# Kernel optimization log

Measured on AMD Instinct MI355X. Metric: run time of the kernel, lower is better.

## Reference

```python
import jax, jax.numpy as jnp
import numpy as np

BETA = 0.5        # membrane decay (from source)
THRESHOLD = 1.0   # snn.Leaky default
ALPHA = 2.0       # ATan surrogate default slope (snntorch)


@jax.custom_vjp
def spike_fn(v):
    # Heaviside spike: 1 where membrane - threshold > 0
    return (v > 0).astype(v.dtype)


def _spike_fwd(v):
    return spike_fn(v), v


def _spike_bwd(v, g):
    # snntorch ATan surrogate gradient: (alpha/2) / (1 + (pi/2*alpha*v)^2)
    grad = (ALPHA / 2.0) / (1.0 + (jnp.pi / 2.0 * ALPHA * v) ** 2)
    return (g * grad,)


spike_fn.defvjp(_spike_fwd, _spike_bwd)


def setup_inputs() -> dict:
    key = jax.random.key(0)
    # x: [T, B, N] = [num_steps, batch, neurons]
    x = jax.random.normal(key, (128, 64, 4096), dtype=jnp.float32)
    return {"x": x}


def reference(x):
    # snntorch Leaky with init_hidden=True, reset_mechanism='subtract':
    #   reset_t = H(mem_{t-1} - thr)
    #   mem_t   = beta*mem_{t-1} + x_t - reset_t*thr
    #   spk_t   = H(mem_t - thr)
    mem0 = jnp.zeros(x.shape[1:], dtype=x.dtype)

    def step(mem, xt):
        reset = spike_fn(mem - THRESHOLD)
        mem_new = BETA * mem + xt - reset * THRESHOLD
        spk = spike_fn(mem_new - THRESHOLD)
        return mem_new, spk

    _, spk_rec = jax.lax.scan(step, mem0, x)  # spk_rec: [T, B, N]
    return spk_rec
```

## Files before the change

### kernel.cpp

```cpp
#include <hip/hip_runtime.h>


#define T_STEPS 128
#define T_HALF 64
#define D 8

__device__ __forceinline__ float4 lif_step(float4& mem, const float4 v) {
    mem.x = 0.5f * mem.x + v.x - (mem.x > 1.0f ? 1.0f : 0.0f);
    mem.y = 0.5f * mem.y + v.y - (mem.y > 1.0f ? 1.0f : 0.0f);
    mem.z = 0.5f * mem.z + v.z - (mem.z > 1.0f ? 1.0f : 0.0f);
    mem.w = 0.5f * mem.w + v.w - (mem.w > 1.0f ? 1.0f : 0.0f);
    float4 s;
    s.x = mem.x > 1.0f ? 1.0f : 0.0f;
    s.y = mem.y > 1.0f ? 1.0f : 0.0f;
    s.z = mem.z > 1.0f ? 1.0f : 0.0f;
    s.w = mem.w > 1.0f ? 1.0f : 0.0f;
    return s;
}

__global__ __launch_bounds__(256) void snn_leaky_fwd(const float4* __restrict__ x,
                                                     float4* __restrict__ out,
                                                     int n4) {
    const int chunk = blockIdx.x & 255;
    const int phase = blockIdx.x >> 8;
    const int col = chunk * 256 + threadIdx.x;

    const float4* xp = x + col;
    float4* op = out + col;

    float4 buf[D];
    float4 mem = make_float4(0.f, 0.f, 0.f, 0.f);

#pragma unroll
    for (int u = 0; u < D; ++u) buf[u] = xp[(size_t)u * n4];

    if (phase == 0) {
#pragma unroll
        for (int t = 0; t < T_HALF; ++t) {
            const float4 v = buf[t % D];
            if (t + D < T_HALF) buf[t % D] = xp[(size_t)(t + D) * n4];
            const float4 s = lif_step(mem, v);
            op[(size_t)t * n4] = s;
        }
    } else {
#pragma unroll
        for (int t = 0; t < T_HALF; ++t) {
            const float4 v = buf[t % D];
            buf[t % D] = xp[(size_t)(t + D) * n4];
            (void)lif_step(mem, v);
        }
#pragma unroll
        for (int t = T_HALF; t < T_STEPS; ++t) {
            const float4 v = buf[t % D];
            if (t + D < T_STEPS) buf[t % D] = xp[(size_t)(t + D) * n4];
            const float4 s = lif_step(mem, v);
            op[(size_t)t * n4] = s;
        }
    }
}

extern "C" void kernel_launch(void* const* d_in, const int* in_sizes, int n_in,
                              void* d_out, int out_size, void* d_ws, size_t ws_size,
                              hipStream_t stream) {
    const float4* x = (const float4*)d_in[0];
    float4* out = (float4*)d_out;

    const int total = in_sizes[0];
    const int n4 = total / T_STEPS / 4;

    snn_leaky_fwd<<<512, 256, 0, stream>>>(x, out, n4);
}
```

Before: 224.4 us.

## Replace split-phase recompute with single pass paced by cross-block atomic barriers

Drops the two-phase scheme, where the second half of blocks re-ran the first 64 timesteps just to rebuild membrane state. Each of 256 blocks now walks all 128 steps. Blocks are held roughly in lockstep every 8 steps by a global atomic counter with bounded spinning, so memory traffic stays time-aligned across the device. This removes the redundant reads and compute, but halves the grid and adds 15 barrier rounds of atomic spinning plus a memset before launch.

```diff
diff --git a/kernel.cpp b/kernel.cpp
--- a/kernel.cpp
+++ b/kernel.cpp
@@ -2,8 +2,12 @@
 
 
 #define T_STEPS 128
-#define T_HALF 64
 #define D 8
+#define KWIN 8
+#define NWIN (T_STEPS / KWIN)
+#define NBLK 256
+#define BLKT 256
+#define SPIN_CAP 20000
 
 __device__ __forceinline__ float4 lif_step(float4& mem, const float4 v) {
     mem.x = 0.5f * mem.x + v.x - (mem.x > 1.0f ? 1.0f : 0.0f);
@@ -18,13 +22,11 @@
     return s;
 }
 
-__global__ __launch_bounds__(256) void snn_leaky_fwd(const float4* __restrict__ x,
-                                                     float4* __restrict__ out,
-                                                     int n4) {
-    const int chunk = blockIdx.x & 255;
-    const int phase = blockIdx.x >> 8;
-    const int col = chunk * 256 + threadIdx.x;
-
+__global__ __launch_bounds__(BLKT) void snn_leaky_fwd(const float4* __restrict__ x,
+                                                      float4* __restrict__ out,
+                                                      unsigned int* __restrict__ pace,
+                                                      int n4) {
+    const int col = blockIdx.x * BLKT + threadIdx.x;
     const float4* xp = x + col;
     float4* op = out + col;
 
@@ -34,27 +36,30 @@
 #pragma unroll
     for (int u = 0; u < D; ++u) buf[u] = xp[(size_t)u * n4];
 
-    if (phase == 0) {
+    for (int w = 0; w < NWIN; ++w) {
 #pragma unroll
-        for (int t = 0; t < T_HALF; ++t) {
-            const float4 v = buf[t % D];
-            if (t + D < T_HALF) buf[t % D] = xp[(size_t)(t + D) * n4];
+        for (int k = 0; k < KWIN; ++k) {
+            const int t = w * KWIN + k;
+            const float4 v = buf[k & (D - 1)];
+            if (t + D < T_STEPS) buf[k & (D - 1)] = xp[(size_t)(t + D) * n4];
             const float4 s = lif_step(mem, v);
             op[(size_t)t * n4] = s;
         }
-    } else {
-#pragma unroll
-        for (int t = 0; t < T_HALF; ++t) {
-            const float4 v = buf[t % D];
-            buf[t % D] = xp[(size_t)(t + D) * n4];
-            (void)lif_step(mem, v);
-        }
-#pragma unroll
-        for (int t = T_HALF; t < T_STEPS; ++t) {
-            const float4 v = buf[t % D];
-            if (t + D < T_STEPS) buf[t % D] = xp[(size_t)(t + D) * n4];
-            const float4 s = lif_step(mem, v);
-            op[(size_t)t * n4] = s;
+        if (w + 1 < NWIN) {
+            if (threadIdx.x == 0) {
+                __hip_atomic_fetch_add(&pace[w], 1u, __ATOMIC_RELAXED,
+                                       __HIP_MEMORY_SCOPE_AGENT);
+                int spins = 0;
+                for (;;) {
+                    const unsigned int seen =
+                        __hip_atomic_load(&pace[w], __ATOMIC_RELAXED,
+                                          __HIP_MEMORY_SCOPE_AGENT);
+                    if (seen >= (unsigned int)NBLK) break;
+                    if (++spins >= SPIN_CAP) break;
+                    __builtin_amdgcn_s_sleep(2);
+                }
+            }
+            __syncthreads();
         }
     }
 }
@@ -68,5 +73,8 @@
     const int total = in_sizes[0];
     const int n4 = total / T_STEPS / 4;
 
-    snn_leaky_fwd<<<512, 256, 0, stream>>>(x, out, n4);
+    unsigned int* pace = (unsigned int*)d_ws;
+    hipMemsetAsync(pace, 0, NWIN * sizeof(unsigned int), stream);
+
+    snn_leaky_fwd<<<NBLK, BLKT, 0, stream>>>(x, out, pace, n4);
 }
```

Measured after the change: 296.5 us. 1.32x slower.

## Drop time-split recompute; give each thread two columns over all timesteps

Applied to the files above, without the earlier changes.

Removes the two-phase scheme. Before, half the blocks re-ran the first 64 timesteps without storing, only to warm up the membrane state for the second half. Now each thread owns a float2 column pair and runs all 128 steps. The same 512 blocks are launched, with float2 accesses instead of float4. The prefetch depth grows from 8 to 16. This removes the redundant re-read of the first half of x, at the cost of narrower per-thread memory accesses.

```diff
diff --git a/kernel.cpp b/kernel.cpp
--- a/kernel.cpp
+++ b/kernel.cpp
@@ -2,71 +2,47 @@
 
 
 #define T_STEPS 128
-#define T_HALF 64
-#define D 8
+#define D 16
 
-__device__ __forceinline__ float4 lif_step(float4& mem, const float4 v) {
+__device__ __forceinline__ float2 lif_step(float2& mem, const float2 v) {
     mem.x = 0.5f * mem.x + v.x - (mem.x > 1.0f ? 1.0f : 0.0f);
     mem.y = 0.5f * mem.y + v.y - (mem.y > 1.0f ? 1.0f : 0.0f);
-    mem.z = 0.5f * mem.z + v.z - (mem.z > 1.0f ? 1.0f : 0.0f);
-    mem.w = 0.5f * mem.w + v.w - (mem.w > 1.0f ? 1.0f : 0.0f);
-    float4 s;
+    float2 s;
     s.x = mem.x > 1.0f ? 1.0f : 0.0f;
     s.y = mem.y > 1.0f ? 1.0f : 0.0f;
-    s.z = mem.z > 1.0f ? 1.0f : 0.0f;
-    s.w = mem.w > 1.0f ? 1.0f : 0.0f;
     return s;
 }
 
-__global__ __launch_bounds__(256) void snn_leaky_fwd(const float4* __restrict__ x,
-                                                     float4* __restrict__ out,
-                                                     int n4) {
-    const int chunk = blockIdx.x & 255;
-    const int phase = blockIdx.x >> 8;
-    const int col = chunk * 256 + threadIdx.x;
+__global__ __launch_bounds__(256) void snn_leaky_fwd(const float2* __restrict__ x,
+                                                     float2* __restrict__ out,
+                                                     int n2) {
+    const int col = blockIdx.x * 256 + threadIdx.x;
+    const float2* xp = x + col;
+    float2* op = out + col;
 
-    const float4* xp = x + col;
-    float4* op = out + col;
-
-    float4 buf[D];
-    float4 mem = make_float4(0.f, 0.f, 0.f, 0.f);
+    float2 buf[D];
+    float2 mem = make_float2(0.f, 0.f);
 
 #pragma unroll
-    for (int u = 0; u < D; ++u) buf[u] = xp[(size_t)u * n4];
+    for (int u = 0; u < D; ++u) buf[u] = xp[(size_t)u * n2];
 
-    if (phase == 0) {
 #pragma unroll
-        for (int t = 0; t < T_HALF; ++t) {
-            const float4 v = buf[t % D];
-            if (t + D < T_HALF) buf[t % D] = xp[(size_t)(t + D) * n4];
-            const float4 s = lif_step(mem, v);
-            op[(size_t)t * n4] = s;
-        }
-    } else {
-#pragma unroll
-        for (int t = 0; t < T_HALF; ++t) {
-            const float4 v = buf[t % D];
-            buf[t % D] = xp[(size_t)(t + D) * n4];
-            (void)lif_step(mem, v);
-        }
-#pragma unroll
-        for (int t = T_HALF; t < T_STEPS; ++t) {
-            const float4 v = buf[t % D];
-            if (t + D < T_STEPS) buf[t % D] = xp[(size_t)(t + D) * n4];
-            const float4 s = lif_step(mem, v);
-            op[(size_t)t * n4] = s;
-        }
+    for (int t = 0; t < T_STEPS; ++t) {
+        const float2 v = buf[t & (D - 1)];
+        if (t + D < T_STEPS) buf[t & (D - 1)] = xp[(size_t)(t + D) * n2];
+        const float2 s = lif_step(mem, v);
+        op[(size_t)t * n2] = s;
     }
 }
 
 extern "C" void kernel_launch(void* const* d_in, const int* in_sizes, int n_in,
                               void* d_out, int out_size, void* d_ws, size_t ws_size,
                               hipStream_t stream) {
-    const float4* x = (const float4*)d_in[0];
-    float4* out = (float4*)d_out;
+    const float2* x = (const float2*)d_in[0];
+    float2* out = (float2*)d_out;
 
     const int total = in_sizes[0];
-    const int n4 = total / T_STEPS / 4;
+    const int n2 = total / T_STEPS / 2;
 
-    snn_leaky_fwd<<<512, 256, 0, stream>>>(x, out, n4);
+    snn_leaky_fwd<<<n2 / 256, 256, 0, stream>>>(x, out, n2);
 }
```

New measurement: 225.2 us. No clear change (+0.3%).

## Split time into four recompute phases and process two columns per thread

Applied to the files above, without the earlier changes.

The time axis is now split into four segments instead of two. Each block replays the membrane recurrence over the prefix steps without storing output, then emits spikes for its own segment. Each thread now handles two float4 columns to add independent work alongside the serial chain. In exchange, redundant prefix reads of x grow noticeably. The loops now have runtime bounds, so the circular buffer is indexed dynamically and risks being moved to scratch memory.

```diff
diff --git a/kernel.cpp b/kernel.cpp
--- a/kernel.cpp
+++ b/kernel.cpp
@@ -2,8 +2,11 @@
 
 
 #define T_STEPS 128
-#define T_HALF 64
+#define P 4
+#define TP (T_STEPS / P)
 #define D 8
+#define BLKT 256
+#define G 2
 
 __device__ __forceinline__ float4 lif_step(float4& mem, const float4 v) {
     mem.x = 0.5f * mem.x + v.x - (mem.x > 1.0f ? 1.0f : 0.0f);
@@ -18,43 +21,44 @@
     return s;
 }
 
-__global__ __launch_bounds__(256) void snn_leaky_fwd(const float4* __restrict__ x,
-                                                     float4* __restrict__ out,
-                                                     int n4) {
-    const int chunk = blockIdx.x & 255;
-    const int phase = blockIdx.x >> 8;
-    const int col = chunk * 256 + threadIdx.x;
+__global__ __launch_bounds__(BLKT) void snn_leaky_fwd(const float4* __restrict__ x,
+                                                      float4* __restrict__ out,
+                                                      int n4) {
+    const int slab  = blockIdx.x & 127;
+    const int phase = blockIdx.x >> 7;
+    const int col0  = slab * (BLKT * G) + threadIdx.x;
+    const float4* xp = x + col0;
+    float4* op = out + col0;
+    const int t_beg = phase * TP;
+    const int t_end = t_beg + TP;
 
-    const float4* xp = x + col;
-    float4* op = out + col;
-
-    float4 buf[D];
-    float4 mem = make_float4(0.f, 0.f, 0.f, 0.f);
+    float4 buf[D][G];
+    float4 mem[G];
+#pragma unroll
+    for (int g = 0; g < G; ++g) mem[g] = make_float4(0.f, 0.f, 0.f, 0.f);
 
 #pragma unroll
-    for (int u = 0; u < D; ++u) buf[u] = xp[(size_t)u * n4];
+    for (int u = 0; u < D; ++u)
+#pragma unroll
+        for (int g = 0; g < G; ++g)
+            buf[u][g] = xp[(size_t)u * n4 + g * BLKT];
 
-    if (phase == 0) {
+    for (int t = 0; t < t_beg; ++t) {
 #pragma unroll
-        for (int t = 0; t < T_HALF; ++t) {
-            const float4 v = buf[t % D];
-            if (t + D < T_HALF) buf[t % D] = xp[(size_t)(t + D) * n4];
-            const float4 s = lif_step(mem, v);
-            op[(size_t)t * n4] = s;
+        for (int g = 0; g < G; ++g) {
+            const float4 v = buf[t & (D - 1)][g];
+            buf[t & (D - 1)][g] = xp[(size_t)(t + D) * n4 + g * BLKT];
+            (void)lif_step(mem[g], v);
         }
-    } else {
+    }
+
+    for (int t = t_beg; t < t_end; ++t) {
 #pragma unroll
-        for (int t = 0; t < T_HALF; ++t) {
-            const float4 v = buf[t % D];
-            buf[t % D] = xp[(size_t)(t + D) * n4];
-            (void)lif_step(mem, v);
-        }
-#pragma unroll
-        for (int t = T_HALF; t < T_STEPS; ++t) {
-            const float4 v = buf[t % D];
-            if (t + D < T_STEPS) buf[t % D] = xp[(size_t)(t + D) * n4];
-            const float4 s = lif_step(mem, v);
-            op[(size_t)t * n4] = s;
+        for (int g = 0; g < G; ++g) {
+            const float4 v = buf[t & (D - 1)][g];
+            if (t + D < t_end) buf[t & (D - 1)][g] = xp[(size_t)(t + D) * n4 + g * BLKT];
+            const float4 s = lif_step(mem[g], v);
+            op[(size_t)t * n4 + g * BLKT] = s;
         }
     }
 }
@@ -68,5 +72,5 @@
     const int total = in_sizes[0];
     const int n4 = total / T_STEPS / 4;
 
-    snn_leaky_fwd<<<512, 256, 0, stream>>>(x, out, n4);
+    snn_leaky_fwd<<<512, BLKT, 0, stream>>>(x, out, n4);
 }
```

Measured after the change: 362.1 us. +61.4%, slower.
